# Kernel optimization log

Hardware: AMD Instinct MI355X
Metric: run time of the kernel (lower is better)

## Reference

```python
import jax, jax.numpy as jnp
import numpy as np

R = 16
EPS = 1e-6
OFFSETS = (1, 2, 4, 8, 16, 32)
_IDX_I, _IDX_J = np.triu_indices(R, k=1)  # plu_dim = 120


def _plucker(u, v):
    # u, v: (B, L, r) -> (B, L, plu_dim), normalized with eps-clamped norm
    p = u[..., _IDX_I] * v[..., _IDX_J] - u[..., _IDX_J] * v[..., _IDX_I]
    norm = jnp.maximum(jnp.linalg.norm(p, axis=-1, keepdims=True), EPS)
    return p / norm


def setup_inputs() -> dict:
    key = jax.random.key(0)
    ks = jax.random.split(key, 6)
    B, L, D, d_geom = 4, 4096, 1024, 256
    plu_dim = R * (R - 1) // 2
    s = lambda fan_in: 1.0 / np.sqrt(fan_in)
    return {
        "h": jax.random.normal(ks[0], (B, L, D), jnp.float32),
        "red_w": jax.random.normal(ks[1], (D, R), jnp.float32) * s(D),
        "red_b": jnp.zeros((R,), jnp.float32),
        "g1_w": jax.random.normal(ks[2], (plu_dim, d_geom), jnp.float32) * s(plu_dim),
        "g1_b": jnp.zeros((d_geom,), jnp.float32),
        "g2_w": jax.random.normal(ks[3], (d_geom, D), jnp.float32) * s(d_geom),
        "g2_b": jnp.zeros((D,), jnp.float32),
        "gate_w": jax.random.normal(ks[4], (2 * D, D), jnp.float32) * s(2 * D),
        "gate_b": jnp.zeros((D,), jnp.float32),
    }


def reference(h, red_w, red_b, g1_w, g1_b, g2_w, g2_b, gate_w, gate_b):
    B, L, D = h.shape
    z = h @ red_w + red_b  # (B, L, r)
    geom_sum = jnp.zeros((B, L, D), h.dtype)
    count = jnp.zeros((B, L, 1), h.dtype)
    pos = jnp.arange(L)
    for delta in OFFSETS:
        if delta >= L:
            continue
        # causal shift: z_past[t] = z[t - delta], zero-padded
        z_past = jnp.pad(z[:, : L - delta], ((0, 0), (delta, 0), (0, 0)))
        p = _plucker(z_past, z)  # (B, L, plu_dim)
        g_delta = jax.nn.gelu(p @ g1_w + g1_b, approximate=False) @ g2_w + g2_b
        mask = (pos >= delta).astype(h.dtype)[None, :, None]  # (1, L, 1)
        geom_sum = geom_sum + g_delta * mask
        count = count + jnp.broadcast_to(mask, (B, L, 1))
    g = geom_sum / jnp.maximum(count, 1.0)
    alpha = jax.nn.sigmoid(jnp.concatenate([h, g], axis=-1) @ gate_w + gate_b)
    return alpha * h + (1.0 - alpha) * g
```

## Files before the change

### kernel.cpp

```cpp
#include <hip/hip_runtime.h>
#include <hip/hip_bf16.h>
#include <math.h>

typedef unsigned short u16;
typedef unsigned int u32;
typedef __attribute__((ext_vector_type(8))) short short8;
typedef __attribute__((ext_vector_type(4))) float f32x4;

#define L_SEQ 4096
#define N_TOK 16384
#define D_MODEL 1024
#define R_DIM 16
#define PLU 120
#define G_DIM 256
#define K_CAT 1536
#define K_GATE 2048

typedef __attribute__((address_space(1))) const void* as1cvp;
typedef __attribute__((address_space(3))) void* as3vp;
#define GLD16(g, l) \
  __builtin_amdgcn_global_load_lds((as1cvp)(g), (as3vp)(l), 16, 0, 0)

#define CFENCE asm volatile("" ::: "memory")
#define BARB                        \
  {                                 \
    CFENCE;                         \
    __builtin_amdgcn_s_barrier();   \
    CFENCE;                         \
  }
#define VM0 asm volatile("s_waitcnt vmcnt(0)" ::: "memory")

__device__ __forceinline__ u16 f2bf(float f) {
  u32 x = __float_as_uint(f);
  u32 lsb = (x >> 16) & 1u;
  x += 0x7fffu + lsb;
  return (u16)(x >> 16);
}
__device__ __forceinline__ float bf2f(u16 u) {
  return __uint_as_float(((u32)u) << 16);
}
__device__ __forceinline__ u32 pack2(float a, float b) {
  return (u32)f2bf(a) | ((u32)f2bf(b) << 16);
}

__device__ __forceinline__ float gelu_erf(float x) {
  const float y = x * 0.70710678118654752f;
  const float a = fabsf(y);
  const float t = __builtin_amdgcn_rcpf(fmaf(0.3275911f, a, 1.0f));
  float poly = fmaf(1.061405429f, t, -1.453152027f);
  poly = fmaf(poly, t, 1.421413741f);
  poly = fmaf(poly, t, -0.284496736f);
  poly = fmaf(poly, t, 0.254829592f);
  poly *= t;
  const float e = __builtin_amdgcn_exp2f(-1.4426950408889634f * a * a);
  float er = fmaf(-poly, e, 1.0f);
  er = copysignf(er, y);
  const float hx = 0.5f * x;
  return fmaf(hx, er, hx);
}

constexpr int PLU_I[PLU] = {
    0, 0, 0, 0, 0, 0, 0, 0, 0, 0, 0, 0, 0, 0, 0,
    1, 1, 1, 1, 1, 1, 1, 1, 1, 1, 1, 1, 1, 1,
    2, 2, 2, 2, 2, 2, 2, 2, 2, 2, 2, 2, 2,
    3, 3, 3, 3, 3, 3, 3, 3, 3, 3, 3, 3,
    4, 4, 4, 4, 4, 4, 4, 4, 4, 4, 4,
    5, 5, 5, 5, 5, 5, 5, 5, 5, 5,
    6, 6, 6, 6, 6, 6, 6, 6, 6,
    7, 7, 7, 7, 7, 7, 7, 7,
    8, 8, 8, 8, 8, 8, 8,
    9, 9, 9, 9, 9, 9,
    10, 10, 10, 10, 10,
    11, 11, 11, 11,
    12, 12, 12,
    13, 13,
    14};
constexpr int PLU_J[PLU] = {
    1, 2, 3, 4, 5, 6, 7, 8, 9, 10, 11, 12, 13, 14, 15,
    2, 3, 4, 5, 6, 7, 8, 9, 10, 11, 12, 13, 14, 15,
    3, 4, 5, 6, 7, 8, 9, 10, 11, 12, 13, 14, 15,
    4, 5, 6, 7, 8, 9, 10, 11, 12, 13, 14, 15,
    5, 6, 7, 8, 9, 10, 11, 12, 13, 14, 15,
    6, 7, 8, 9, 10, 11, 12, 13, 14, 15,
    7, 8, 9, 10, 11, 12, 13, 14, 15,
    8, 9, 10, 11, 12, 13, 14, 15,
    9, 10, 11, 12, 13, 14, 15,
    10, 11, 12, 13, 14, 15,
    11, 12, 13, 14, 15,
    12, 13, 14, 15,
    13, 14, 15,
    14, 15,
    15};

__global__ __launch_bounds__(256) void k_cvtT(const float* __restrict__ src,
                                              u16* __restrict__ dst, int K,
                                              int Kp, int N) {
  __shared__ float t[32][33];
  const int k0 = blockIdx.y * 32, n0 = blockIdx.x * 32;
  const int r = threadIdx.x >> 3, c4 = (threadIdx.x & 7) * 4;
  float4 v = {0.f, 0.f, 0.f, 0.f};
  if (k0 + r < K) v = *(const float4*)(src + (size_t)(k0 + r) * N + n0 + c4);
  t[r][c4] = v.x;
  t[r][c4 + 1] = v.y;
  t[r][c4 + 2] = v.z;
  t[r][c4 + 3] = v.w;
  __syncthreads();
  uint2 o;
  o.x = pack2(t[c4][r], t[c4 + 1][r]);
  o.y = pack2(t[c4 + 2][r], t[c4 + 3][r]);
  *(uint2*)(dst + (size_t)(n0 + r) * Kp + k0 + c4) = o;
}

__global__ __launch_bounds__(256) void k_reduce(const float* __restrict__ h,
                                                const float* __restrict__ red_w,
                                                const float* __restrict__ red_b,
                                                float* __restrict__ z,
                                                u16* __restrict__ hb) {
  __shared__ alignas(16) u16 hs[16 * D_MODEL];
  const int tid = threadIdx.x;
  const int t0 = blockIdx.x * 16;

  const float4* src = (const float4*)(h + (size_t)t0 * D_MODEL);
  u32* dst = (u32*)hs;
#pragma unroll
  for (int it = 0; it < (16 * D_MODEL / 4) / 256; ++it) {
    const int idx = tid + it * 256;
    const float4 v = src[idx];
    dst[idx * 2 + 0] = pack2(v.x, v.y);
    dst[idx * 2 + 1] = pack2(v.z, v.w);
  }
  __syncthreads();

  {
    const uint4* s4 = (const uint4*)hs;
    uint4* d4 = (uint4*)(hb + (size_t)t0 * D_MODEL);
#pragma unroll
    for (int it = 0; it < (16 * D_MODEL / 8) / 256; ++it)
      d4[tid + it * 256] = s4[tid + it * 256];
  }

  const int m = tid >> 4, c = tid & 15;
  const u16* hrow = hs + m * D_MODEL;
  float acc = 0.f;
#pragma unroll 8
  for (int i = 0; i < D_MODEL; i += 2) {
    u32 hv = *(const u32*)(hrow + i);
    float h0 = __uint_as_float(hv << 16);
    float h1 = __uint_as_float(hv & 0xffff0000u);
    acc = fmaf(h0, red_w[i * R_DIM + c], acc);
    acc = fmaf(h1, red_w[(i + 1) * R_DIM + c], acc);
  }
  z[(size_t)(t0 + m) * R_DIM + c] = acc + red_b[c];
}

#define PLUG(G)                                                               \
  _Pragma("unroll") for (int cc = 0; cc < 2; ++cc) {                          \
    u32 ow[4];                                                                \
    _Pragma("unroll") for (int eo = 0; eo < 4; ++eo) {                        \
      float pp[2];                                                            \
      _Pragma("unroll") for (int e2 = 0; e2 < 2; ++e2) {                      \
        const int k = ((G)*2 + cc) * 8 + eo * 2 + e2;                         \
        float p = 0.f;                                                        \
        if (k < PLU) {                                                        \
          p = zp[PLU_I[k]] * zcr[PLU_J[k]] - zp[PLU_J[k]] * zcr[PLU_I[k]];    \
          s = fmaf(p, p, s);                                                  \
        }                                                                     \
        pp[e2] = p;                                                           \
      }                                                                       \
      ow[eo] = pack2(pp[0], pp[1]);                                           \
    }                                                                         \
    *(uint4*)&pb[((((G)*2 + cc) ^ rsw) * 8)] = *(uint4*)ow;                   \
  }

__global__ __launch_bounds__(512) void k_plu(const float* __restrict__ z,
                                             const u16* __restrict__ W1t,
                                             const float* __restrict__ g1b,
                                             u16* __restrict__ A, int t0g) {
  __shared__ alignas(16) float zx[96][17];
  __shared__ alignas(16) u16 W1s[128][128];
  __shared__ alignas(16) u16 Pb[64][128];
  __shared__ float prt[64][8];
  __shared__ float rno[64];
  __shared__ float b1s[128];

  const int tid = threadIdx.x, lane = tid & 63, w = tid >> 6;
  const int wm = w >> 2, wn = w & 3;
  const int n0 = blockIdx.x * 128;
  const int tl = blockIdx.y * 64;
  const int tg = t0g + tl;
  const int l0 = tg & (L_SEQ - 1);
  const int mr = lane & 15;
  const int qlane = lane >> 4;

  if (tid < 128) b1s[tid] = g1b[n0 + tid];
  for (int r = tid; r < 96 * 16; r += 512) {
    const int rr = r >> 4, c = r & 15;
    int t = tg - 32 + rr;
    if (t < 0) t = 0;
    zx[rr][c] = z[(size_t)t * R_DIM + c];
  }
  {
    const uint4* src = (const uint4*)(W1t + (size_t)n0 * 128);
    for (int i = tid; i < 128 * 16; i += 512) {
      const int r = i >> 4, c = i & 15;
      *(uint4*)&W1s[r][(c ^ (r & 15)) * 8] = src[i];
    }
  }
  __syncthreads();

  float zcr[R_DIM];
  {
    const float* zc = zx[32 + lane];
#pragma unroll
    for (int c = 0; c < R_DIM; ++c) zcr[c] = zc[c];
  }

  f32x4 acc[2][2];

#pragma unroll 1
  for (int dd = 0; dd < 6; ++dd) {
    const int delta = 1 << dd;
    if (dd) __syncthreads();
    {
      const int row = lane;
      const int rsw = lane & 15;
      const float* zpr = zx[32 + row - delta];
      float zp[R_DIM];
#pragma unroll
      for (int c = 0; c < R_DIM; ++c) zp[c] = zpr[c];
      float s = 0.f;
      u16* pb = &Pb[row][0];
      switch (w) {
        case 0: PLUG(0); break;
        case 1: PLUG(1); break;
        case 2: PLUG(2); break;
        case 3: PLUG(3); break;
        case 4: PLUG(4); break;
        case 5: PLUG(5); break;
        case 6: PLUG(6); break;
        default: PLUG(7); break;
      }
      prt[row][w] = s;
    }
    __syncthreads();
    if (tid < 64) {
      const float s = prt[tid][0] + prt[tid][1] + prt[tid][2] + prt[tid][3] +
                      prt[tid][4] + prt[tid][5] + prt[tid][6] + prt[tid][7];
      rno[tid] = 1.0f / fmaxf(sqrtf(s), 1e-6f);
    }
    __syncthreads();
#pragma unroll
    for (int a = 0; a < 2; ++a)
#pragma unroll
      for (int b = 0; b < 2; ++b) acc[a][b] = (f32x4)(0.f);
#pragma unroll
    for (int k0 = 0; k0 < 128; k0 += 32) {
      const int ci = (k0 >> 3) + qlane;
      short8 af[2], bfr[2];
#pragma unroll
      for (int mi = 0; mi < 2; ++mi) {
        const int r = wm * 32 + mi * 16 + mr;
        af[mi] = *(const short8*)&Pb[r][(ci ^ (r & 15)) * 8];
      }
#pragma unroll
      for (int ni = 0; ni < 2; ++ni) {
        const int r = wn * 32 + ni * 16 + mr;
        bfr[ni] = *(const short8*)&W1s[r][(ci ^ (r & 15)) * 8];
      }
#pragma unroll
      for (int mi = 0; mi < 2; ++mi)
#pragma unroll
        for (int ni = 0; ni < 2; ++ni)
          acc[mi][ni] = __builtin_amdgcn_mfma_f32_16x16x32_bf16(
              af[mi], bfr[ni], acc[mi][ni], 0, 0, 0);
    }
#pragma unroll
    for (int mi = 0; mi < 2; ++mi) {
#pragma unroll
      for (int r = 0; r < 4; ++r) {
        const int rowl = wm * 32 + mi * 16 + qlane * 4 + r;
        const bool ok = (l0 + rowl) >= delta;
        const float rn = rno[rowl];
#pragma unroll
        for (int ni = 0; ni < 2; ++ni) {
          const int colL = wn * 32 + ni * 16 + mr;
          const float x = acc[mi][ni][r] * rn + b1s[colL];
          const float ge = gelu_erf(x);
          A[(size_t)(tl + rowl) * K_CAT + dd * G_DIM + n0 + colL] =
              ok ? f2bf(ge) : (u16)0;
        }
      }
    }
  }
}


#define COMP(BUF)                                                             \
  {                                                                           \
    _Pragma("unroll") for (int kk = 0; kk < 2; ++kk) {                        \
      short8 af[4], bfr[4];                                                   \
      _Pragma("unroll") for (int mi = 0; mi < 4; ++mi) {                      \
        const int r = wm * 64 + mi * 16 + mr;                                 \
        af[mi] = *(const short8*)&lds[(BUF)*8192 + r * 64 +                   \
                                      (((qlane + kk * 4) ^ (r & 7)) << 3)];   \
      }                                                                       \
      _Pragma("unroll") for (int ni = 0; ni < 4; ++ni) {                      \
        const int r = wn * 64 + ni * 16 + mr;                                 \
        bfr[ni] = *(const short8*)&lds[16384 + (BUF)*8192 + r * 64 +          \
                                       (((qlane + kk * 4) ^ (r & 7)) << 3)];  \
      }                                                                       \
      _Pragma("unroll") for (int mi = 0; mi < 4; ++mi)                        \
          _Pragma("unroll") for (int ni = 0; ni < 4; ++ni) acc[mi][ni] =      \
          __builtin_amdgcn_mfma_f32_16x16x32_bf16(af[mi], bfr[ni],            \
                                                  acc[mi][ni], 0, 0, 0);      \
    }                                                                         \
  }

__global__ __launch_bounds__(256, 2) void k_gemm2(const u16* __restrict__ A,
                                                  const u16* __restrict__ W2t,
                                                  const float* __restrict__ g2b,
                                                  u16* __restrict__ g,
                                                  int t0g) {
  __shared__ alignas(16) u16 lds[32768];
  const int tid = threadIdx.x, lane = tid & 63, w = tid >> 6;
  const int wm = w >> 1, wn = w & 1;

  const int cpx = (int)gridDim.x >> 3;
  const int wi = ((int)blockIdx.x & 7) * cpx + ((int)blockIdx.x >> 3);
  const int n0 = (wi & 7) << 7;
  const int ml = (wi >> 3) << 7;

  const int lr3 = lane >> 3, lc = lane & 7;
  const int koff = (lc ^ lr3) << 3;
  const int rb = w * 32 + lr3;
  const u16* a0 = A + (size_t)(ml + rb) * K_CAT + koff;
  const u16* b0 = W2t + (size_t)(n0 + rb) * G_DIM + koff;

#define STA(BUF, T)                                                           \
  _Pragma("unroll") for (int q = 0; q < 4; ++q)                               \
      GLD16(a0 + (size_t)(q * 8) * K_CAT + (T)*64,                            \
            lds + (BUF)*8192 + (w * 32 + q * 8) * 64);
#define STB(BUF, T)                                                           \
  _Pragma("unroll") for (int q = 0; q < 4; ++q)                               \
      GLD16(b0 + (size_t)(q * 8) * G_DIM + (((T)*64) & (G_DIM - 1)),          \
            lds + 16384 + (BUF)*8192 + (w * 32 + q * 8) * 64);

  const int qlane = lane >> 4, mr = lane & 15;

  f32x4 acc[4][4];
#pragma unroll
  for (int a = 0; a < 4; ++a)
#pragma unroll
    for (int b = 0; b < 4; ++b) acc[a][b] = (f32x4)(0.f);

  const int NT = K_CAT / 64;
  STA(0, 0);
  STB(0, 0);
  VM0;
  BARB;
#pragma unroll 1
  for (int i = 0; i < NT / 2; ++i) {
    const int t1 = 2 * i + 1;
    STA(1, t1);
    STB(1, t1);
    COMP(0);
    VM0;
    BARB;
    const bool pf = (t1 + 1 < NT);
    if (pf) {
      STA(0, t1 + 1);
      STB(0, t1 + 1);
    }
    COMP(1);
    if (pf) {
      VM0;
      BARB;
    }
  }

  const int colb = n0 + wn * 64 + mr;
#pragma unroll
  for (int mi = 0; mi < 4; ++mi) {
#pragma unroll
    for (int r = 0; r < 4; ++r) {
      const int rowl = ml + wm * 64 + mi * 16 + qlane * 4 + r;
      const int l = (t0g + rowl) & (L_SEQ - 1);
      const float cnt = (float)((l >= 1) + (l >= 2) + (l >= 4) + (l >= 8) +
                                (l >= 16) + (l >= 32));
      const float inv = 1.0f / fmaxf(cnt, 1.0f);
#pragma unroll
      for (int ni = 0; ni < 4; ++ni) {
        const int col = colb + ni * 16;
        const float v = (acc[mi][ni][r] + cnt * g2b[col]) * inv;
        g[(size_t)rowl * D_MODEL + col] = f2bf(v);
      }
    }
  }
#undef STA
#undef STB
}

__global__ __launch_bounds__(256, 2) void k_gate(const u16* __restrict__ hb,
                                                 const u16* __restrict__ g,
                                                 const u16* __restrict__ WtG,
                                                 const float* __restrict__ gb,
                                                 float* __restrict__ out,
                                                 int t0g) {
  __shared__ alignas(16) u16 lds[32768];
  const int tid = threadIdx.x, lane = tid & 63, w = tid >> 6;
  const int wm = w >> 1, wn = w & 1;

  const int cpx = (int)gridDim.x >> 3;
  const int wi = ((int)blockIdx.x & 7) * cpx + ((int)blockIdx.x >> 3);
  const int n0 = (wi & 7) << 7;
  const int ml = (wi >> 3) << 7;

  const int lr3 = lane >> 3, lc = lane & 7;
  const int koff = (lc ^ lr3) << 3;
  const int rb = w * 32 + lr3;
  const u16* ph = hb + (size_t)(t0g + ml + rb) * D_MODEL + koff;
  const u16* pg = g + (size_t)(ml + rb) * D_MODEL + koff;
  const u16* pb = WtG + (size_t)(n0 + rb) * K_GATE + koff;

#define STA(BUF, T)                                                           \
  {                                                                           \
    const u16* s_ = ((T) < 16 ? ph : pg) + (size_t)((T)&15) * 64;             \
    _Pragma("unroll") for (int q = 0; q < 4; ++q)                             \
        GLD16(s_ + (size_t)(q * 8) * D_MODEL,                                 \
              lds + (BUF)*8192 + (w * 32 + q * 8) * 64);                      \
  }
#define STB(BUF, T)                                                           \
  _Pragma("unroll") for (int q = 0; q < 4; ++q)                               \
      GLD16(pb + (size_t)(q * 8) * K_GATE + (T)*64,                           \
            lds + 16384 + (BUF)*8192 + (w * 32 + q * 8) * 64);

  const int qlane = lane >> 4, mr = lane & 15;

  f32x4 acc[4][4];
#pragma unroll
  for (int a = 0; a < 4; ++a)
#pragma unroll
    for (int b = 0; b < 4; ++b) acc[a][b] = (f32x4)(0.f);

  const int NT = K_GATE / 64;
  STA(0, 0);
  STB(0, 0);
  VM0;
  BARB;
#pragma unroll 1
  for (int i = 0; i < NT / 2; ++i) {
    const int t1 = 2 * i + 1;
    STA(1, t1);
    STB(1, t1);
    COMP(0);
    VM0;
    BARB;
    const bool pf = (t1 + 1 < NT);
    if (pf) {
      STA(0, t1 + 1);
      STB(0, t1 + 1);
    }
    COMP(1);
    if (pf) {
      VM0;
      BARB;
    }
  }

  const int colb = n0 + wn * 64 + mr;
#pragma unroll
  for (int mi = 0; mi < 4; ++mi) {
#pragma unroll
    for (int r = 0; r < 4; ++r) {
      const int rowl = ml + wm * 64 + mi * 16 + qlane * 4 + r;
      const size_t rowg = (size_t)(t0g + rowl) * D_MODEL;
#pragma unroll
      for (int ni = 0; ni < 4; ++ni) {
        const int col = colb + ni * 16;
        const float x = acc[mi][ni][r] + gb[col];
        const float al = 1.0f / (1.0f + expf(-x));
        const float hv = bf2f(hb[rowg + col]);
        const float gv = bf2f(g[(size_t)rowl * D_MODEL + col]);
        out[rowg + col] = fmaf(al, hv - gv, gv);
      }
    }
  }
#undef STA
#undef STB
}

extern "C" void kernel_launch(void* const* d_in, const int* in_sizes, int n_in,
                              void* d_out, int out_size, void* d_ws,
                              size_t ws_size, hipStream_t stream) {
  const float* h = (const float*)d_in[0];
  const float* red_w = (const float*)d_in[1];
  const float* red_b = (const float*)d_in[2];
  const float* g1w = (const float*)d_in[3];
  const float* g1b = (const float*)d_in[4];
  const float* g2w = (const float*)d_in[5];
  const float* g2b = (const float*)d_in[6];
  const float* gate_w = (const float*)d_in[7];
  const float* gate_b = (const float*)d_in[8];
  float* out = (float*)d_out;

  const size_t sz_z = ((size_t)N_TOK * R_DIM * 4 + 255) & ~(size_t)255;
  const size_t sz_hb = (size_t)N_TOK * D_MODEL * 2;
  const size_t sz_WtG = (size_t)D_MODEL * K_GATE * 2;
  const size_t sz_W2t = (size_t)D_MODEL * G_DIM * 2;
  const size_t sz_W1t = (size_t)G_DIM * 128 * 2;
  const size_t fixed = sz_z + sz_hb + sz_WtG + sz_W2t + sz_W1t + 4096;

  int nc = 1;
  for (; nc <= 8; nc *= 2) {
    const size_t ct = N_TOK / nc;
    if (fixed + ct * (size_t)K_CAT * 2 + ct * (size_t)D_MODEL * 2 <= ws_size)
      break;
  }
  if (nc > 8) nc = 8;
  const int ct = N_TOK / nc;

  char* p = (char*)d_ws;
  float* z = (float*)p;
  p += sz_z;
  u16* hb = (u16*)p;
  p += sz_hb;
  u16* WtG = (u16*)p;
  p += sz_WtG;
  u16* W2t = (u16*)p;
  p += sz_W2t;
  u16* W1t = (u16*)p;
  p += sz_W1t;
  u16* Abuf = (u16*)p;
  p += (size_t)ct * K_CAT * 2;
  u16* gbuf = (u16*)p;

  k_reduce<<<dim3(N_TOK / 16), 256, 0, stream>>>(h, red_w, red_b, z, hb);
  k_cvtT<<<dim3(G_DIM / 32, 128 / 32), 256, 0, stream>>>(g1w, W1t, PLU, 128,
                                                         G_DIM);
  k_cvtT<<<dim3(D_MODEL / 32, G_DIM / 32), 256, 0, stream>>>(g2w, W2t, G_DIM,
                                                             G_DIM, D_MODEL);
  k_cvtT<<<dim3(D_MODEL / 32, K_GATE / 32), 256, 0, stream>>>(
      gate_w, WtG, K_GATE, K_GATE, D_MODEL);

  for (int c = 0; c < nc; ++c) {
    const int t0g = c * ct;
    k_plu<<<dim3(2, ct / 64), 512, 0, stream>>>(z, W1t, g1b, Abuf, t0g);
    k_gemm2<<<dim3((ct / 128) * 8), 256, 0, stream>>>(Abuf, W2t, g2b, gbuf,
                                                      t0g);
    k_gate<<<dim3((ct / 128) * 8), 256, 0, stream>>>(hb, gbuf, WtG, gate_b,
                                                     out, t0g);
  }
}
```

Measured before the change: 337.8 us.

## Single-buffer LDS in gemm2 and gate kernels to raise occupancy

```diff
diff --git a/kernel.cpp b/kernel.cpp
--- a/kernel.cpp
+++ b/kernel.cpp
@@ -295,18 +295,18 @@
 }
 
 
-#define COMP(BUF)                                                             \
+#define COMP                                                                  \
   {                                                                           \
     _Pragma("unroll") for (int kk = 0; kk < 2; ++kk) {                        \
       short8 af[4], bfr[4];                                                   \
       _Pragma("unroll") for (int mi = 0; mi < 4; ++mi) {                      \
         const int r = wm * 64 + mi * 16 + mr;                                 \
-        af[mi] = *(const short8*)&lds[(BUF)*8192 + r * 64 +                   \
+        af[mi] = *(const short8*)&lds[r * 64 +                                \
                                       (((qlane + kk * 4) ^ (r & 7)) << 3)];   \
       }                                                                       \
       _Pragma("unroll") for (int ni = 0; ni < 4; ++ni) {                      \
         const int r = wn * 64 + ni * 16 + mr;                                 \
-        bfr[ni] = *(const short8*)&lds[16384 + (BUF)*8192 + r * 64 +          \
+        bfr[ni] = *(const short8*)&lds[8192 + r * 64 +                        \
                                        (((qlane + kk * 4) ^ (r & 7)) << 3)];  \
       }                                                                       \
       _Pragma("unroll") for (int mi = 0; mi < 4; ++mi)                        \
@@ -316,12 +316,12 @@
     }                                                                         \
   }
 
-__global__ __launch_bounds__(256, 2) void k_gemm2(const u16* __restrict__ A,
+__global__ __launch_bounds__(256, 4) void k_gemm2(const u16* __restrict__ A,
                                                   const u16* __restrict__ W2t,
                                                   const float* __restrict__ g2b,
                                                   u16* __restrict__ g,
                                                   int t0g) {
-  __shared__ alignas(16) u16 lds[32768];
+  __shared__ alignas(16) u16 lds[16384];
   const int tid = threadIdx.x, lane = tid & 63, w = tid >> 6;
   const int wm = w >> 1, wn = w & 1;
 
@@ -336,14 +336,14 @@
   const u16* a0 = A + (size_t)(ml + rb) * K_CAT + koff;
   const u16* b0 = W2t + (size_t)(n0 + rb) * G_DIM + koff;
 
-#define STA(BUF, T)                                                           \
+#define STA(T)                                                                \
   _Pragma("unroll") for (int q = 0; q < 4; ++q)                               \
       GLD16(a0 + (size_t)(q * 8) * K_CAT + (T)*64,                            \
-            lds + (BUF)*8192 + (w * 32 + q * 8) * 64);
-#define STB(BUF, T)                                                           \
+            lds + (w * 32 + q * 8) * 64);
+#define STB(T)                                                                \
   _Pragma("unroll") for (int q = 0; q < 4; ++q)                               \
       GLD16(b0 + (size_t)(q * 8) * G_DIM + (((T)*64) & (G_DIM - 1)),          \
-            lds + 16384 + (BUF)*8192 + (w * 32 + q * 8) * 64);
+            lds + 8192 + (w * 32 + q * 8) * 64);
 
   const int qlane = lane >> 4, mr = lane & 15;
 
@@ -354,25 +354,17 @@
     for (int b = 0; b < 4; ++b) acc[a][b] = (f32x4)(0.f);
 
   const int NT = K_CAT / 64;
-  STA(0, 0);
-  STB(0, 0);
+  STA(0);
+  STB(0);
   VM0;
   BARB;
 #pragma unroll 1
-  for (int i = 0; i < NT / 2; ++i) {
-    const int t1 = 2 * i + 1;
-    STA(1, t1);
-    STB(1, t1);
-    COMP(0);
-    VM0;
-    BARB;
-    const bool pf = (t1 + 1 < NT);
-    if (pf) {
-      STA(0, t1 + 1);
-      STB(0, t1 + 1);
-    }
-    COMP(1);
-    if (pf) {
+  for (int t = 0; t < NT; ++t) {
+    COMP;
+    if (t + 1 < NT) {
+      BARB;
+      STA(t + 1);
+      STB(t + 1);
       VM0;
       BARB;
     }
@@ -400,13 +392,13 @@
 #undef STB
 }
 
-__global__ __launch_bounds__(256, 2) void k_gate(const u16* __restrict__ hb,
+__global__ __launch_bounds__(256, 4) void k_gate(const u16* __restrict__ hb,
                                                  const u16* __restrict__ g,
                                                  const u16* __restrict__ WtG,
                                                  const float* __restrict__ gb,
                                                  float* __restrict__ out,
                                                  int t0g) {
-  __shared__ alignas(16) u16 lds[32768];
+  __shared__ alignas(16) u16 lds[16384];
   const int tid = threadIdx.x, lane = tid & 63, w = tid >> 6;
   const int wm = w >> 1, wn = w & 1;
 
@@ -422,17 +414,17 @@
   const u16* pg = g + (size_t)(ml + rb) * D_MODEL + koff;
   const u16* pb = WtG + (size_t)(n0 + rb) * K_GATE + koff;
 
-#define STA(BUF, T)                                                           \
+#define STA(T)                                                                \
   {                                                                           \
     const u16* s_ = ((T) < 16 ? ph : pg) + (size_t)((T)&15) * 64;             \
     _Pragma("unroll") for (int q = 0; q < 4; ++q)                             \
         GLD16(s_ + (size_t)(q * 8) * D_MODEL,                                 \
-              lds + (BUF)*8192 + (w * 32 + q * 8) * 64);                      \
-  }
-#define STB(BUF, T)                                                           \
+              lds + (w * 32 + q * 8) * 64);                                   \
+  }
+#define STB(T)                                                                \
   _Pragma("unroll") for (int q = 0; q < 4; ++q)                               \
       GLD16(pb + (size_t)(q * 8) * K_GATE + (T)*64,                           \
-            lds + 16384 + (BUF)*8192 + (w * 32 + q * 8) * 64);
+            lds + 8192 + (w * 32 + q * 8) * 64);
 
   const int qlane = lane >> 4, mr = lane & 15;
 
@@ -443,25 +435,17 @@
     for (int b = 0; b < 4; ++b) acc[a][b] = (f32x4)(0.f);
 
   const int NT = K_GATE / 64;
-  STA(0, 0);
-  STB(0, 0);
+  STA(0);
+  STB(0);
   VM0;
   BARB;
 #pragma unroll 1
-  for (int i = 0; i < NT / 2; ++i) {
-    const int t1 = 2 * i + 1;
-    STA(1, t1);
-    STB(1, t1);
-    COMP(0);
-    VM0;
-    BARB;
-    const bool pf = (t1 + 1 < NT);
-    if (pf) {
-      STA(0, t1 + 1);
-      STB(0, t1 + 1);
-    }
-    COMP(1);
-    if (pf) {
+  for (int t = 0; t < NT; ++t) {
+    COMP;
+    if (t + 1 < NT) {
+      BARB;
+      STA(t + 1);
+      STB(t + 1);
       VM0;
       BARB;
     }
```

Measured after the change: 339.3 us. Within noise of the previous version (+0.4%).
